# Kernel optimization log

Hardware: AMD Instinct MI355X
Metric: run time of the kernel (lower is better)

The kernel has to match this reference:

```python
import jax, jax.numpy as jnp
import numpy as np
from jax import lax

E = 8      # embed dim
H = 8      # num heads (head_dim = 1)
EPS = 1e-5


def pe_row(pos, d=E):
    # PositionalEncoding quirk: original adds pe[:, x.size(1), :] -> a SINGLE row at index L.
    i = jnp.arange(0, d, 2, dtype=jnp.float32)
    div = jnp.exp(i * (-np.log(10000.0) / d))
    row = jnp.zeros((d,), jnp.float32)
    row = row.at[0::2].set(jnp.sin(pos * div))
    row = row.at[1::2].set(jnp.cos(pos * div))
    return row


def layernorm(x, g, b):
    mu = jnp.mean(x, axis=-1, keepdims=True)
    var = jnp.mean((x - mu) ** 2, axis=-1, keepdims=True)
    return (x - mu) / jnp.sqrt(var + EPS) * g + b


def mha(q, k, v, wi, bi, wo, bo):
    # torch nn.MultiheadAttention, batch_first, eval mode (dropout off)
    d = E // H
    qp = q @ wi[:E].T + bi[:E]
    kp = k @ wi[E:2 * E].T + bi[E:2 * E]
    vp = v @ wi[2 * E:].T + bi[2 * E:]
    sh = lambda x: x.reshape(x.shape[0], x.shape[1], H, d).transpose(0, 2, 1, 3)
    qh, kh, vh = sh(qp), sh(kp), sh(vp)
    scores = jnp.einsum('bhqd,bhkd->bhqk', qh, kh) / np.sqrt(d)
    attn = jax.nn.softmax(scores, axis=-1)
    o = jnp.einsum('bhqk,bhkd->bhqd', attn, vh)
    B, _, L, _ = o.shape
    o = o.transpose(0, 2, 1, 3).reshape(B, L, E)
    return o @ wo.T + bo


def conv1d_k1p1(x, w, b):
    # Conv1d kernel_size=1, padding=1 (conv_tgt branch), then permute to (B, L, C)
    y = lax.conv_general_dilated(x, w, (1,), [(1, 1)],
                                 dimension_numbers=('NCW', 'OIW', 'NCW'))
    return (y + b[None, :, None]).transpose(0, 2, 1)


def setup_inputs() -> dict:
    key = jax.random.key(0)
    ks = jax.random.split(key, 32)
    B = 8192
    r = lambda i, shape, s=0.05: jax.random.normal(ks[i], shape, jnp.float32) * s
    return {
        'eeg': jax.random.normal(ks[0], (B, 2, 20, 118), jnp.float32),
        'pupil': jax.random.normal(ks[1], (B, 2, 30), jnp.float32),
        'speech': jax.random.normal(ks[2], (B, 2, 30), jnp.float32),
        'action': jax.random.normal(ks[3], (B, 2, 30), jnp.float32),
        'location': jax.random.normal(ks[4], (B, 3, 30), jnp.float32),
        'tgt': jax.random.normal(ks[5], (B, 30), jnp.float32),
        'eeg_conv_w': r(6, (E, 2, 20, 2), 0.1), 'eeg_conv_b': r(7, (E,)),
        'psa_conv_w': r(8, (E, 2, 1), 0.3), 'psa_conv_b': r(9, (E,)),
        'loc_conv_w': r(10, (E, 3, 1), 0.3), 'loc_conv_b': r(11, (E,)),
        'tgt_conv_w': r(12, (E, 1, 1), 0.3), 'tgt_conv_b': r(13, (E,)),
        'norm_g': jnp.ones((E,), jnp.float32), 'norm_b': jnp.zeros((E,), jnp.float32),
        'cross_in_w': r(14, (3 * E, E), 0.3), 'cross_in_b': r(15, (3 * E,)),
        'cross_out_w': r(16, (E, E), 0.3), 'cross_out_b': r(17, (E,)),
        'self_in_w': r(18, (3 * E, E), 0.3), 'self_in_b': r(19, (3 * E,)),
        'self_out_w': r(20, (E, E), 0.3), 'self_out_b': r(21, (E,)),
        'out_in_w': r(22, (3 * E, E), 0.3), 'out_in_b': r(23, (3 * E,)),
        'out_out_w': r(24, (E, E), 0.3), 'out_out_b': r(25, (E,)),
        'fc1_w': r(26, (90, 256), 0.1), 'fc1_b': r(27, (90,)),
    }


def reference(eeg, pupil, speech, action, location, tgt,
              eeg_conv_w, eeg_conv_b, psa_conv_w, psa_conv_b,
              loc_conv_w, loc_conv_b, tgt_conv_w, tgt_conv_b,
              norm_g, norm_b,
              cross_in_w, cross_in_b, cross_out_w, cross_out_b,
              self_in_w, self_in_b, self_out_w, self_out_b,
              out_in_w, out_in_b, out_out_w, out_out_b,
              fc1_w, fc1_b):
    B = eeg.shape[0]
    # eeg conv2d: (B,2,20,118) -> (B,8,1,30) -> (B,30,8)
    e = lax.conv_general_dilated(eeg, eeg_conv_w, (1, 4), 'VALID',
                                 dimension_numbers=('NCHW', 'OIHW', 'NCHW'))
    e = (e + eeg_conv_b[None, :, None, None]).squeeze(2).transpose(0, 2, 1)
    # pupil/speech/action/location (raw len 30 -> conv_tgt branch -> seq 32)
    p = conv1d_k1p1(pupil, psa_conv_w, psa_conv_b)
    s = conv1d_k1p1(speech, psa_conv_w, psa_conv_b)
    a = conv1d_k1p1(action, psa_conv_w, psa_conv_b)
    l = conv1d_k1p1(location, loc_conv_w, loc_conv_b)
    # positional encoding adds single row pe[L]
    e = e + pe_row(30.0)
    p = p + pe_row(32.0)
    s = s + pe_row(32.0)
    a = a + pe_row(32.0)
    l = l + pe_row(32.0)

    cross = lambda q, kv: mha(q, kv, kv, cross_in_w, cross_in_b, cross_out_w, cross_out_b)
    selfa = lambda x: mha(x, x, x, self_in_w, self_in_b, self_out_w, self_out_b)
    nrm = lambda x: layernorm(x, norm_g, norm_b)

    eeg_final = (nrm(cross(e, p)) + nrm(cross(e, a)) + nrm(cross(e, l))
                 + nrm(selfa(e)) + nrm(cross(e, s)))
    pupil_final = (nrm(cross(p, e)) + nrm(cross(p, a)) + nrm(cross(p, l))
                   + nrm(selfa(p)) + nrm(cross(p, s)))
    s_cross_l = nrm(cross(s, l))
    speech_final = (nrm(cross(s, e)) + nrm(cross(s, p)) + nrm(cross(s, a))
                    + s_cross_l)  # original omits speech_self
    # original bug: action_cross_location = norm(speech_cross_location)
    action_final = (nrm(cross(a, e)) + nrm(cross(a, p)) + s_cross_l
                    + nrm(selfa(a)) + nrm(cross(a, s)))
    concatenated = jnp.concatenate([eeg_final, pupil_final, action_final, speech_final], axis=1)  # (B,126,8)

    t = conv1d_k1p1(tgt[:, None, :], tgt_conv_w, tgt_conv_b)  # (B,32,8)
    t = t + pe_row(32.0)
    out = mha(t, concatenated, concatenated, out_in_w, out_in_b, out_out_w, out_out_b)  # (B,32,8)
    out = out.reshape(B, 32 * E) @ fc1_w.T + fc1_b  # (B,90)
    out = out.reshape(B, 30, 3).transpose(0, 2, 1)  # (B,3,30)
    return jax.nn.softmax(out, axis=1)
```

## Files before the change

### kernel.cpp

```cpp
#include <hip/hip_runtime.h>
#include <cstdint>
#include <cstddef>

#define NT 256
#define LOG2E 1.4426950408889634f

typedef float v2f __attribute__((ext_vector_type(2)));
typedef float v4f __attribute__((ext_vector_type(4)));

#if defined(__has_builtin)
#  if __has_builtin(__builtin_amdgcn_exp2f)
#    define EXP2F(x) __builtin_amdgcn_exp2f(x)
#  else
#    define EXP2F(x) exp2f(x)
#  endif
#else
#  define EXP2F(x) exp2f(x)
#endif

enum {
  OFF_EEGB = 0,
  OFF_PSAW = 8,
  OFF_PSAB = 24,
  OFF_LOCW = 32,
  OFF_LOCB = 56,
  OFF_TGTW = 64,
  OFF_TGTB = 72,
  OFF_NG   = 80,
  OFF_NB   = 88,
  OFF_CINW = 96,
  OFF_CINB = 288,
  OFF_COUTW= 312,
  OFF_COUTB= 376,
  OFF_SINW = 384,
  OFF_SINB = 576,
  OFF_SOUTW= 600,
  OFF_SOUTB= 664,
  OFF_OINW = 672,
  OFF_OINB = 864,
  OFF_OOUTW= 888,
  OFF_OOUTB= 952,
  OFF_FC1B = 960,
  OFF_PE30 = 1052,
  OFF_PE32 = 1060,
  OFF_Ebuf = 1068,
  OFF_Pbuf = 1308,
  OFF_Sbuf = 1564,
  OFF_Abuf = 1820,
  OFF_Lbuf = 2076,
  OFF_Tbuf = 2332,
  OFF_CAT  = 2588,
  OFF_QP   = 3596,
  OFF_K8   = 4236,
  OFF_V8   = 6540,
  OFF_FCO  = 8844,
  SM_TOTAL = 8936,
  OFF_EEGW = OFF_K8,
  OFF_KF   = OFF_K8,
  OFF_VF   = OFF_K8 + 1056,
};


__device__ __forceinline__ float grp8_sum(float v) {
  v += __shfl_xor(v, 1);
  v += __shfl_xor(v, 2);
  v += __shfl_xor(v, 4);
  return v;
}

__device__ __forceinline__ float dot8(const float* __restrict__ x,
                                      const float* __restrict__ w, float bias) {
  v4f xa = *(const v4f*)x, xb = *(const v4f*)(x + 4);
  v4f p = xa * *(const v4f*)w;
  p += xb * *(const v4f*)(w + 4);
  v2f q = p.xy + p.zw;
  return bias + q.x + q.y;
}

template<int LK>
__device__ __forceinline__ void kvproj(int set, int src, int winO, int binO,
                                       float* __restrict__ sm, int tid) {
  if (tid < LK * 8) {
    int r = tid >> 3, hh = tid & 7;
    const float* x = sm + src + r * 8;
    float kk = dot8(x, sm + winO + 64 + hh * 8, sm[binO + 8 + hh]);
    float vv = dot8(x, sm + winO + 128 + hh * 8, sm[binO + 16 + hh]);
    sm[OFF_K8 + set * 288 + hh * 36 + r] = kk;
    sm[OFF_V8 + set * 288 + hh * 36 + r] = vv;
  }
}

template<int LK>
__device__ __forceinline__ float attn_nv(float q, int qi, int h, int set,
                                         int woutO, int boutO, float* __restrict__ sm) {
  const float* Kp = sm + OFF_K8 + set * 288 + h * 36;
  const float* Vp = sm + OFF_V8 + set * 288 + h * 36;
  v4f l4 = {0.f,0.f,0.f,0.f}, A4 = {0.f,0.f,0.f,0.f};
  #pragma unroll
  for (int t = 0; t < (LK >> 2); t++) {
    v4f kk = *(const v4f*)(Kp + 4 * t);
    v4f vv = *(const v4f*)(Vp + 4 * t);
    v4f sc = kk * q;
    v4f ee = { EXP2F(sc.x), EXP2F(sc.y), EXP2F(sc.z), EXP2F(sc.w) };
    l4 += ee; A4 += ee * vv;
  }
  if constexpr ((LK & 3) != 0) {
    v2f kk = *(const v2f*)(Kp + (LK & ~3));
    v2f vv = *(const v2f*)(Vp + (LK & ~3));
    v2f sc = kk * q;
    v2f ee = { EXP2F(sc.x), EXP2F(sc.y) };
    l4.xy = l4.xy + ee; A4.xy = A4.xy + ee * vv;
  }
  v2f lp = l4.xy + l4.zw, ap = A4.xy + A4.zw;
  float ov = (ap.x + ap.y) * __builtin_amdgcn_rcpf(lp.x + lp.y);
  sm[OFF_QP + qi * 20 + h] = ov;
  float a = dot8(sm + OFF_QP + qi * 20, sm + woutO + h * 8, sm[boutO + h]);
  float mu = grp8_sum(a) * 0.125f;
  float dd = a - mu;
  return fmaf(dd * rsqrtf(grp8_sum(dd * dd) * 0.125f + 1e-5f),
              sm[OFF_NG + h], sm[OFF_NB + h]);
}

__global__ __launch_bounds__(NT, 4) void cmt_kernel(
    const float* __restrict__ eeg, const float* __restrict__ pupil,
    const float* __restrict__ speech, const float* __restrict__ action,
    const float* __restrict__ location, const float* __restrict__ tgt,
    const float* __restrict__ eeg_w, const float* __restrict__ eeg_b,
    const float* __restrict__ psa_w, const float* __restrict__ psa_b,
    const float* __restrict__ loc_w, const float* __restrict__ loc_b,
    const float* __restrict__ tgt_w, const float* __restrict__ tgt_b,
    const float* __restrict__ ng, const float* __restrict__ nb,
    const float* __restrict__ cin_w, const float* __restrict__ cin_b,
    const float* __restrict__ cout_w, const float* __restrict__ cout_b,
    const float* __restrict__ sin_w, const float* __restrict__ sin_b,
    const float* __restrict__ sout_w, const float* __restrict__ sout_b,
    const float* __restrict__ oin_w, const float* __restrict__ oin_b,
    const float* __restrict__ oout_w, const float* __restrict__ oout_b,
    const float* __restrict__ fc1_w, const float* __restrict__ fc1_b,
    float* __restrict__ out)
{
  __shared__ __align__(16) float sm[SM_TOTAL];
  const int tid = threadIdx.x;
  const int b = blockIdx.x;

#define CP(off, p, n) for (int i = tid; i < (n); i += NT) sm[(off)+i] = (p)[i]
#define CPQ(off, p, n, nq) for (int i = tid; i < (n); i += NT) sm[(off)+i] = (p)[i] * ((i < (nq)) ? LOG2E : 1.0f)

  for (int i = tid; i < 640; i += NT) sm[OFF_EEGW + (i / 80) * 84 + (i % 80)] = eeg_w[i];
  CP(OFF_EEGB, eeg_b, 8);
  CP(OFF_PSAW, psa_w, 16);   CP(OFF_PSAB, psa_b, 8);
  CP(OFF_LOCW, loc_w, 24);   CP(OFF_LOCB, loc_b, 8);
  CP(OFF_TGTW, tgt_w, 8);    CP(OFF_TGTB, tgt_b, 8);
  CP(OFF_NG, ng, 8);         CP(OFF_NB, nb, 8);
  CPQ(OFF_CINW, cin_w, 192, 64);  CPQ(OFF_CINB, cin_b, 24, 8);
  CP(OFF_COUTW, cout_w, 64); CP(OFF_COUTB, cout_b, 8);
  CPQ(OFF_SINW, sin_w, 192, 64);  CPQ(OFF_SINB, sin_b, 24, 8);
  CP(OFF_SOUTW, sout_w, 64); CP(OFF_SOUTB, sout_b, 8);
  CPQ(OFF_OINW, oin_w, 192, 64);  CPQ(OFF_OINB, oin_b, 24, 8);
  CP(OFF_OOUTW, oout_w, 64); CP(OFF_OOUTB, oout_b, 8);
  CP(OFF_FC1B, fc1_b, 90);
  if (tid < 16) {
    const float divs[4] = {1.f, 0.1f, 0.01f, 0.001f};
    float pos = (tid < 8) ? 30.f : 32.f;
    int e = tid & 7;
    float x = pos * divs[e >> 1];
    float v = (e & 1) ? cosf(x) : sinf(x);
    sm[((tid < 8) ? OFF_PE30 : OFF_PE32) + e] = v;
  }
  __syncthreads();

  if (tid < 240) {
    int w = tid >> 3, o = tid & 7;
    const float* ep = eeg + (size_t)b * 4720 + 4 * w;
    const float* wr = sm + OFF_EEGW + o * 84;
    v4f acc4 = {0.f, 0.f, 0.f, 0.f};
    #pragma unroll
    for (int t = 0; t < 20; t++) {
      int ik0 = 2 * t, ik1 = 2 * t + 1;
      float2 x0 = *(const float2*)(ep + (ik0 / 20) * 2360 + (ik0 % 20) * 118);
      float2 x1 = *(const float2*)(ep + (ik1 / 20) * 2360 + (ik1 % 20) * 118);
      v4f xv = {x0.x, x0.y, x1.x, x1.y};
      acc4 += xv * *(const v4f*)(wr + 4 * t);
    }
    v2f s2 = acc4.xy + acc4.zw;
    sm[OFF_Ebuf + w * 8 + o] = s2.x + s2.y + sm[OFF_EEGB + o] + sm[OFF_PE30 + o];
  }
  {
    int t = tid >> 3, o = tid & 7;
    bool inb = (t >= 1 && t <= 30);
    int ti = t - 1;
    float pe = sm[OFF_PE32 + o];
    float w0 = sm[OFF_PSAW + 2 * o], w1 = sm[OFF_PSAW + 2 * o + 1];
    float pb = sm[OFF_PSAB + o];
    float vp = pb, vs = pb, va = pb;
    float vl = sm[OFF_LOCB + o], vt = sm[OFF_TGTB + o];
    if (inb) {
      const float* pp = pupil    + (size_t)b * 60 + ti;
      const float* sp = speech   + (size_t)b * 60 + ti;
      const float* ap = action   + (size_t)b * 60 + ti;
      const float* lp = location + (size_t)b * 90 + ti;
      vp = fmaf(pp[0], w0, fmaf(pp[30], w1, vp));
      vs = fmaf(sp[0], w0, fmaf(sp[30], w1, vs));
      va = fmaf(ap[0], w0, fmaf(ap[30], w1, va));
      vl = fmaf(lp[0],  sm[OFF_LOCW + 3 * o],     vl);
      vl = fmaf(lp[30], sm[OFF_LOCW + 3 * o + 1], vl);
      vl = fmaf(lp[60], sm[OFF_LOCW + 3 * o + 2], vl);
      vt = fmaf(tgt[(size_t)b * 30 + ti], sm[OFF_TGTW + o], vt);
    }
    sm[OFF_Pbuf + tid] = vp + pe;
    sm[OFF_Sbuf + tid] = vs + pe;
    sm[OFF_Abuf + tid] = va + pe;
    sm[OFF_Lbuf + tid] = vl + pe;
    sm[OFF_Tbuf + tid] = vt + pe;
  }
  __syncthreads();

  kvproj<30>(0, OFF_Ebuf, OFF_CINW, OFF_CINB, sm, tid);
  kvproj<32>(1, OFF_Pbuf, OFF_CINW, OFF_CINB, sm, tid);
  kvproj<32>(2, OFF_Sbuf, OFF_CINW, OFF_CINB, sm, tid);
  kvproj<32>(3, OFF_Abuf, OFF_CINW, OFF_CINB, sm, tid);
  kvproj<32>(4, OFF_Lbuf, OFF_CINW, OFF_CINB, sm, tid);
  kvproj<30>(5, OFF_Ebuf, OFF_SINW, OFF_SINB, sm, tid);
  kvproj<32>(6, OFF_Pbuf, OFF_SINW, OFF_SINB, sm, tid);
  kvproj<32>(7, OFF_Abuf, OFF_SINW, OFF_SINB, sm, tid);
  __syncthreads();

  const int qi = tid >> 3, h = tid & 7;
  float carry;
  {
    if (qi < 30) {
      const float* xr = sm + OFF_Ebuf + qi * 8;
      float qc = dot8(xr, sm + OFF_CINW + h * 8, sm[OFF_CINB + h]);
      float qs = dot8(xr, sm + OFF_SINW + h * 8, sm[OFF_SINB + h]);
      float cat = attn_nv<32>(qc, qi, h, 1, OFF_COUTW, OFF_COUTB, sm)
                + attn_nv<32>(qc, qi, h, 3, OFF_COUTW, OFF_COUTB, sm)
                + attn_nv<32>(qc, qi, h, 4, OFF_COUTW, OFF_COUTB, sm)
                + attn_nv<30>(qs, qi, h, 5, OFF_SOUTW, OFF_SOUTB, sm)
                + attn_nv<32>(qc, qi, h, 2, OFF_COUTW, OFF_COUTB, sm);
      sm[OFF_CAT + qi * 8 + h] = cat;
    }
    {
      const float* xr = sm + OFF_Pbuf + qi * 8;
      float qc = dot8(xr, sm + OFF_CINW + h * 8, sm[OFF_CINB + h]);
      float qs = dot8(xr, sm + OFF_SINW + h * 8, sm[OFF_SINB + h]);
      float cat = attn_nv<30>(qc, qi, h, 0, OFF_COUTW, OFF_COUTB, sm)
                + attn_nv<32>(qc, qi, h, 3, OFF_COUTW, OFF_COUTB, sm)
                + attn_nv<32>(qc, qi, h, 4, OFF_COUTW, OFF_COUTB, sm)
                + attn_nv<32>(qs, qi, h, 6, OFF_SOUTW, OFF_SOUTB, sm)
                + attn_nv<32>(qc, qi, h, 2, OFF_COUTW, OFF_COUTB, sm);
      sm[OFF_CAT + (30 + qi) * 8 + h] = cat;
    }
    {
      const float* xr = sm + OFF_Sbuf + qi * 8;
      float qc = dot8(xr, sm + OFF_CINW + h * 8, sm[OFF_CINB + h]);
      float n1 = attn_nv<30>(qc, qi, h, 0, OFF_COUTW, OFF_COUTB, sm);
      float n2 = attn_nv<32>(qc, qi, h, 1, OFF_COUTW, OFF_COUTB, sm);
      float n3 = attn_nv<32>(qc, qi, h, 3, OFF_COUTW, OFF_COUTB, sm);
      carry    = attn_nv<32>(qc, qi, h, 4, OFF_COUTW, OFF_COUTB, sm);
      sm[OFF_CAT + (94 + qi) * 8 + h] = n1 + n2 + n3 + carry;
    }
    {
      const float* xr = sm + OFF_Abuf + qi * 8;
      float qc = dot8(xr, sm + OFF_CINW + h * 8, sm[OFF_CINB + h]);
      float qs = dot8(xr, sm + OFF_SINW + h * 8, sm[OFF_SINB + h]);
      float cat = attn_nv<30>(qc, qi, h, 0, OFF_COUTW, OFF_COUTB, sm)
                + attn_nv<32>(qc, qi, h, 1, OFF_COUTW, OFF_COUTB, sm)
                + carry
                + attn_nv<32>(qs, qi, h, 7, OFF_SOUTW, OFF_SOUTB, sm)
                + attn_nv<32>(qc, qi, h, 2, OFF_COUTW, OFF_COUTB, sm);
      sm[OFF_CAT + (62 + qi) * 8 + h] = cat;
    }
  }
  __syncthreads();

  for (int j = tid; j < 1008; j += NT) {
    int r = j >> 3, hh = j & 7;
    const float* x = sm + OFF_CAT + r * 8;
    float kk = dot8(x, sm + OFF_OINW + 64 + hh * 8, sm[OFF_OINB + 8 + hh]);
    float vv = dot8(x, sm + OFF_OINW + 128 + hh * 8, sm[OFF_OINB + 16 + hh]);
    sm[OFF_KF + hh * 132 + r] = kk;
    sm[OFF_VF + hh * 132 + r] = vv;
  }
  __syncthreads();

  {
    float qf = dot8(sm + OFF_Tbuf + qi * 8, sm + OFF_OINW + h * 8, sm[OFF_OINB + h]);
    const float* Kp = sm + OFF_KF + h * 132;
    const float* Vp = sm + OFF_VF + h * 132;
    v4f l4 = {0.f,0.f,0.f,0.f}, A4 = {0.f,0.f,0.f,0.f};
    #pragma unroll
    for (int t = 0; t < 31; t++) {
      v4f kk = *(const v4f*)(Kp + 4 * t);
      v4f vv = *(const v4f*)(Vp + 4 * t);
      v4f sc = kk * qf;
      v4f ee = { EXP2F(sc.x), EXP2F(sc.y), EXP2F(sc.z), EXP2F(sc.w) };
      l4 += ee; A4 += ee * vv;
    }
    {
      v2f kk = *(const v2f*)(Kp + 124);
      v2f vv = *(const v2f*)(Vp + 124);
      v2f sc = kk * qf;
      v2f ee = { EXP2F(sc.x), EXP2F(sc.y) };
      l4.xy = l4.xy + ee; A4.xy = A4.xy + ee * vv;
    }
    v2f lp = l4.xy + l4.zw, ap = A4.xy + A4.zw;
    float ov = (ap.x + ap.y) * __builtin_amdgcn_rcpf(lp.x + lp.y);
    sm[OFF_QP + qi * 20 + h] = ov;
    float a = dot8(sm + OFF_QP + qi * 20, sm + OFF_OOUTW + h * 8, sm[OFF_OOUTB + h]);
    sm[OFF_Tbuf + qi * 8 + h] = a;
  }
  __syncthreads();

  if (tid < 180) {
    int j = tid >> 1, p = tid & 1;
    const v4f* w4 = (const v4f*)(fc1_w + j * 256);
    const v4f* o4 = (const v4f*)(sm + OFF_Tbuf);
    v4f acc4 = {0.f, 0.f, 0.f, 0.f};
    #pragma unroll 8
    for (int c = p; c < 64; c += 2) acc4 += o4[c] * w4[c];
    v2f a2 = acc4.xy + acc4.zw;
    float acc = a2.x + a2.y;
    acc += __shfl_xor(acc, 1);
    if (p == 0) sm[OFF_FCO + j] = acc + sm[OFF_FC1B + j];
  }
  __syncthreads();
  if (tid < 30) {
    float x0 = sm[OFF_FCO + 3 * tid], x1 = sm[OFF_FCO + 3 * tid + 1], x2 = sm[OFF_FCO + 3 * tid + 2];
    float m = fmaxf(x0, fmaxf(x1, x2));
    float e0 = __expf(x0 - m), e1 = __expf(x1 - m), e2 = __expf(x2 - m);
    float inv = __builtin_amdgcn_rcpf(e0 + e1 + e2);
    float* op = out + (size_t)b * 90;
    op[tid]      = e0 * inv;
    op[30 + tid] = e1 * inv;
    op[60 + tid] = e2 * inv;
  }
#undef CP
#undef CPQ
}

extern "C" void kernel_launch(void* const* d_in, const int* in_sizes, int n_in,
                              void* d_out, int out_size, void* d_ws, size_t ws_size,
                              hipStream_t stream) {
  (void)n_in; (void)out_size; (void)d_ws; (void)ws_size;
  int B = in_sizes[0] / 4720;
  cmt_kernel<<<B, NT, 0, stream>>>(
      (const float*)d_in[0],  (const float*)d_in[1],  (const float*)d_in[2],
      (const float*)d_in[3],  (const float*)d_in[4],  (const float*)d_in[5],
      (const float*)d_in[6],  (const float*)d_in[7],  (const float*)d_in[8],
      (const float*)d_in[9],  (const float*)d_in[10], (const float*)d_in[11],
      (const float*)d_in[12], (const float*)d_in[13], (const float*)d_in[14],
      (const float*)d_in[15], (const float*)d_in[16], (const float*)d_in[17],
      (const float*)d_in[18], (const float*)d_in[19], (const float*)d_in[20],
      (const float*)d_in[21], (const float*)d_in[22], (const float*)d_in[23],
      (const float*)d_in[24], (const float*)d_in[25], (const float*)d_in[26],
      (const float*)d_in[27], (const float*)d_in[28], (const float*)d_in[29],
      (float*)d_out);
}
```

Measured before the change: 251.0 us.

## Process two queries per thread to share K/V loads across attention blocks

```diff
diff --git a/kernel.cpp b/kernel.cpp
--- a/kernel.cpp
+++ b/kernel.cpp
@@ -60,65 +60,63 @@
   OFF_VF   = OFF_K8 + 1056,
 };
 
-
-__device__ __forceinline__ float grp8_sum(float v) {
-  v += __shfl_xor(v, 1);
-  v += __shfl_xor(v, 2);
-  v += __shfl_xor(v, 4);
-  return v;
+__device__ __forceinline__ float hsum4(v4f a) {
+  v2f t = a.xy + a.zw;
+  return t.x + t.y;
 }
 
-__device__ __forceinline__ float dot8(const float* __restrict__ x,
-                                      const float* __restrict__ w, float bias) {
-  v4f xa = *(const v4f*)x, xb = *(const v4f*)(x + 4);
-  v4f p = xa * *(const v4f*)w;
-  p += xb * *(const v4f*)(w + 4);
-  v2f q = p.xy + p.zw;
-  return bias + q.x + q.y;
-}
-
 template<int LK>
-__device__ __forceinline__ void kvproj(int set, int src, int winO, int binO,
-                                       float* __restrict__ sm, int tid) {
-  if (tid < LK * 8) {
-    int r = tid >> 3, hh = tid & 7;
-    const float* x = sm + src + r * 8;
-    float kk = dot8(x, sm + winO + 64 + hh * 8, sm[binO + 8 + hh]);
-    float vv = dot8(x, sm + winO + 128 + hh * 8, sm[binO + 16 + hh]);
-    sm[OFF_K8 + set * 288 + hh * 36 + r] = kk;
-    sm[OFF_V8 + set * 288 + hh * 36 + r] = vv;
-  }
-}
-
-template<int LK>
-__device__ __forceinline__ float attn_nv(float q, int qi, int h, int set,
-                                         int woutO, int boutO, float* __restrict__ sm) {
-  const float* Kp = sm + OFF_K8 + set * 288 + h * 36;
-  const float* Vp = sm + OFF_V8 + set * 288 + h * 36;
-  v4f l4 = {0.f,0.f,0.f,0.f}, A4 = {0.f,0.f,0.f,0.f};
+__device__ __forceinline__ void attn2_core(float q1, float q2,
+                                           const float* Kp, const float* Vp,
+                                           float& ov1, float& ov2) {
+  v4f la = {0.f,0.f,0.f,0.f}, Aa = la, lb = la, Ab = la;
   #pragma unroll
   for (int t = 0; t < (LK >> 2); t++) {
     v4f kk = *(const v4f*)(Kp + 4 * t);
     v4f vv = *(const v4f*)(Vp + 4 * t);
-    v4f sc = kk * q;
-    v4f ee = { EXP2F(sc.x), EXP2F(sc.y), EXP2F(sc.z), EXP2F(sc.w) };
-    l4 += ee; A4 += ee * vv;
+    v4f s1 = kk * q1, s2 = kk * q2;
+    v4f e1 = { EXP2F(s1.x), EXP2F(s1.y), EXP2F(s1.z), EXP2F(s1.w) };
+    v4f e2 = { EXP2F(s2.x), EXP2F(s2.y), EXP2F(s2.z), EXP2F(s2.w) };
+    la += e1; Aa += e1 * vv;
+    lb += e2; Ab += e2 * vv;
   }
   if constexpr ((LK & 3) != 0) {
     v2f kk = *(const v2f*)(Kp + (LK & ~3));
     v2f vv = *(const v2f*)(Vp + (LK & ~3));
-    v2f sc = kk * q;
-    v2f ee = { EXP2F(sc.x), EXP2F(sc.y) };
-    l4.xy = l4.xy + ee; A4.xy = A4.xy + ee * vv;
-  }
-  v2f lp = l4.xy + l4.zw, ap = A4.xy + A4.zw;
-  float ov = (ap.x + ap.y) * __builtin_amdgcn_rcpf(lp.x + lp.y);
-  sm[OFF_QP + qi * 20 + h] = ov;
-  float a = dot8(sm + OFF_QP + qi * 20, sm + woutO + h * 8, sm[boutO + h]);
-  float mu = grp8_sum(a) * 0.125f;
-  float dd = a - mu;
-  return fmaf(dd * rsqrtf(grp8_sum(dd * dd) * 0.125f + 1e-5f),
-              sm[OFF_NG + h], sm[OFF_NB + h]);
+    v2f s1 = kk * q1, s2 = kk * q2;
+    v2f e1 = { EXP2F(s1.x), EXP2F(s1.y) };
+    v2f e2 = { EXP2F(s2.x), EXP2F(s2.y) };
+    la.xy = la.xy + e1; Aa.xy = Aa.xy + e1 * vv;
+    lb.xy = lb.xy + e2; Ab.xy = Ab.xy + e2 * vv;
+  }
+  ov1 = hsum4(Aa) * __builtin_amdgcn_rcpf(hsum4(la));
+  ov2 = hsum4(Ab) * __builtin_amdgcn_rcpf(hsum4(lb));
+}
+
+template<int LK>
+__device__ __forceinline__ void attn2_nv(float q1, float q2,
+                                         const float* Kp, const float* Vp,
+                                         float* qslot, int h,
+                                         v4f woa, v4f wob, float bo, float gg, float bb,
+                                         float& nv1, float& nv2) {
+  float ov1, ov2;
+  attn2_core<LK>(q1, q2, Kp, Vp, ov1, ov2);
+  qslot[h] = ov1; qslot[8 + h] = ov2;
+  v4f c0 = *(const v4f*)qslot,       c1 = *(const v4f*)(qslot + 4);
+  v4f d0 = *(const v4f*)(qslot + 8), d1 = *(const v4f*)(qslot + 12);
+  float a1 = bo + hsum4(c0 * woa + c1 * wob);
+  float a2 = bo + hsum4(d0 * woa + d1 * wob);
+  qslot[h] = a1; qslot[8 + h] = a2;
+  c0 = *(const v4f*)qslot;       c1 = *(const v4f*)(qslot + 4);
+  d0 = *(const v4f*)(qslot + 8); d1 = *(const v4f*)(qslot + 12);
+  float mu1 = hsum4(c0 + c1) * 0.125f;
+  float mu2 = hsum4(d0 + d1) * 0.125f;
+  v4f e0 = c0 - mu1, e1v = c1 - mu1;
+  v4f f0 = d0 - mu2, f1v = d1 - mu2;
+  float var1 = hsum4(e0 * e0 + e1v * e1v) * 0.125f;
+  float var2 = hsum4(f0 * f0 + f1v * f1v) * 0.125f;
+  nv1 = fmaf((a1 - mu1) * rsqrtf(var1 + 1e-5f), gg, bb);
+  nv2 = fmaf((a2 - mu2) * rsqrtf(var2 + 1e-5f), gg, bb);
 }
 
 __global__ __launch_bounds__(NT, 4) void cmt_kernel(
@@ -215,99 +213,177 @@
   }
   __syncthreads();
 
-  kvproj<30>(0, OFF_Ebuf, OFF_CINW, OFF_CINB, sm, tid);
-  kvproj<32>(1, OFF_Pbuf, OFF_CINW, OFF_CINB, sm, tid);
-  kvproj<32>(2, OFF_Sbuf, OFF_CINW, OFF_CINB, sm, tid);
-  kvproj<32>(3, OFF_Abuf, OFF_CINW, OFF_CINB, sm, tid);
-  kvproj<32>(4, OFF_Lbuf, OFF_CINW, OFF_CINB, sm, tid);
-  kvproj<30>(5, OFF_Ebuf, OFF_SINW, OFF_SINB, sm, tid);
-  kvproj<32>(6, OFF_Pbuf, OFF_SINW, OFF_SINB, sm, tid);
-  kvproj<32>(7, OFF_Abuf, OFF_SINW, OFF_SINB, sm, tid);
-  __syncthreads();
-
-  const int qi = tid >> 3, h = tid & 7;
-  float carry;
+  const int g = tid >> 3, h = tid & 7;
+  float* qslot = sm + OFF_QP + g * 20;
+
   {
-    if (qi < 30) {
-      const float* xr = sm + OFF_Ebuf + qi * 8;
-      float qc = dot8(xr, sm + OFF_CINW + h * 8, sm[OFF_CINB + h]);
-      float qs = dot8(xr, sm + OFF_SINW + h * 8, sm[OFF_SINB + h]);
-      float cat = attn_nv<32>(qc, qi, h, 1, OFF_COUTW, OFF_COUTB, sm)
-                + attn_nv<32>(qc, qi, h, 3, OFF_COUTW, OFF_COUTB, sm)
-                + attn_nv<32>(qc, qi, h, 4, OFF_COUTW, OFF_COUTB, sm)
-                + attn_nv<30>(qs, qi, h, 5, OFF_SOUTW, OFF_SOUTB, sm)
-                + attn_nv<32>(qc, qi, h, 2, OFF_COUTW, OFF_COUTB, sm);
-      sm[OFF_CAT + qi * 8 + h] = cat;
+    const int r = g;
+    v4f cka = *(const v4f*)(sm + OFF_CINW + 64 + h * 8), ckb = *(const v4f*)(sm + OFF_CINW + 68 + h * 8);
+    v4f cva = *(const v4f*)(sm + OFF_CINW + 128 + h * 8), cvb = *(const v4f*)(sm + OFF_CINW + 132 + h * 8);
+    float cbk = sm[OFF_CINB + 8 + h], cbv = sm[OFF_CINB + 16 + h];
+#define KV1(srcO, set, wka, wkb, wva, wvb, bk, bv) { \
+    v4f xa = *(const v4f*)(sm + (srcO) + r * 8); \
+    v4f xb = *(const v4f*)(sm + (srcO) + r * 8 + 4); \
+    sm[OFF_K8 + (set) * 288 + h * 36 + r] = (bk) + hsum4(xa * (wka) + xb * (wkb)); \
+    sm[OFF_V8 + (set) * 288 + h * 36 + r] = (bv) + hsum4(xa * (wva) + xb * (wvb)); }
+    if (r < 30) KV1(OFF_Ebuf, 0, cka, ckb, cva, cvb, cbk, cbv);
+    KV1(OFF_Pbuf, 1, cka, ckb, cva, cvb, cbk, cbv);
+    KV1(OFF_Sbuf, 2, cka, ckb, cva, cvb, cbk, cbv);
+    KV1(OFF_Abuf, 3, cka, ckb, cva, cvb, cbk, cbv);
+    KV1(OFF_Lbuf, 4, cka, ckb, cva, cvb, cbk, cbv);
+    v4f ska = *(const v4f*)(sm + OFF_SINW + 64 + h * 8), skb = *(const v4f*)(sm + OFF_SINW + 68 + h * 8);
+    v4f sva = *(const v4f*)(sm + OFF_SINW + 128 + h * 8), svb = *(const v4f*)(sm + OFF_SINW + 132 + h * 8);
+    float sbk = sm[OFF_SINB + 8 + h], sbv = sm[OFF_SINB + 16 + h];
+    if (r < 30) KV1(OFF_Ebuf, 5, ska, skb, sva, svb, sbk, sbv);
+    KV1(OFF_Pbuf, 6, ska, skb, sva, svb, sbk, sbv);
+    KV1(OFF_Abuf, 7, ska, skb, sva, svb, sbk, sbv);
+#undef KV1
+  }
+  __syncthreads();
+
+#define KSET(s) (sm + OFF_K8 + (s) * 288 + h * 36)
+#define VSET(s) (sm + OFF_V8 + (s) * 288 + h * 36)
+  {
+    v4f qwc_a = *(const v4f*)(sm + OFF_CINW + h * 8), qwc_b = *(const v4f*)(sm + OFF_CINW + h * 8 + 4);
+    v4f woc_a = *(const v4f*)(sm + OFF_COUTW + h * 8), woc_b = *(const v4f*)(sm + OFF_COUTW + h * 8 + 4);
+    float bqc = sm[OFF_CINB + h], boc = sm[OFF_COUTB + h];
+    float gg = sm[OFF_NG + h], bb = sm[OFF_NB + h];
+    float t1, t2;
+
+    if (g < 16) {
+      {
+        const float* x1 = sm + OFF_Ebuf + g * 8;
+        const float* x2 = sm + OFF_Ebuf + ((g < 14) ? (g + 16) : 13) * 8;
+        v4f x1a = *(const v4f*)x1, x1b = *(const v4f*)(x1 + 4);
+        v4f x2a = *(const v4f*)x2, x2b = *(const v4f*)(x2 + 4);
+        float qc1 = bqc + hsum4(x1a * qwc_a + x1b * qwc_b);
+        float qc2 = bqc + hsum4(x2a * qwc_a + x2b * qwc_b);
+        float cat1, cat2;
+        attn2_nv<32>(qc1, qc2, KSET(1), VSET(1), qslot, h, woc_a, woc_b, boc, gg, bb, cat1, cat2);
+        attn2_nv<32>(qc1, qc2, KSET(3), VSET(3), qslot, h, woc_a, woc_b, boc, gg, bb, t1, t2);
+        cat1 += t1; cat2 += t2;
+        attn2_nv<32>(qc1, qc2, KSET(4), VSET(4), qslot, h, woc_a, woc_b, boc, gg, bb, t1, t2);
+        cat1 += t1; cat2 += t2;
+        {
+          v4f qws_a = *(const v4f*)(sm + OFF_SINW + h * 8), qws_b = *(const v4f*)(sm + OFF_SINW + h * 8 + 4);
+          v4f wos_a = *(const v4f*)(sm + OFF_SOUTW + h * 8), wos_b = *(const v4f*)(sm + OFF_SOUTW + h * 8 + 4);
+          float qs1 = sm[OFF_SINB + h] + hsum4(x1a * qws_a + x1b * qws_b);
+          float qs2 = sm[OFF_SINB + h] + hsum4(x2a * qws_a + x2b * qws_b);
+          attn2_nv<30>(qs1, qs2, KSET(5), VSET(5), qslot, h, wos_a, wos_b, sm[OFF_SOUTB + h], gg, bb, t1, t2);
+          cat1 += t1; cat2 += t2;
+        }
+        attn2_nv<32>(qc1, qc2, KSET(2), VSET(2), qslot, h, woc_a, woc_b, boc, gg, bb, t1, t2);
+        cat1 += t1; cat2 += t2;
+        sm[OFF_CAT + g * 8 + h] = cat1;
+        if (g < 14) sm[OFF_CAT + (g + 16) * 8 + h] = cat2;
+      }
+      {
+        const float* x1 = sm + OFF_Pbuf + g * 8;
+        const float* x2 = sm + OFF_Pbuf + (g + 16) * 8;
+        v4f x1a = *(const v4f*)x1, x1b = *(const v4f*)(x1 + 4);
+        v4f x2a = *(const v4f*)x2, x2b = *(const v4f*)(x2 + 4);
+        float qc1 = bqc + hsum4(x1a * qwc_a + x1b * qwc_b);
+        float qc2 = bqc + hsum4(x2a * qwc_a + x2b * qwc_b);
+        float cat1, cat2;
+        attn2_nv<30>(qc1, qc2, KSET(0), VSET(0), qslot, h, woc_a, woc_b, boc, gg, bb, cat1, cat2);
+        attn2_nv<32>(qc1, qc2, KSET(3), VSET(3), qslot, h, woc_a, woc_b, boc, gg, bb, t1, t2);
+        cat1 += t1; cat2 += t2;
+        attn2_nv<32>(qc1, qc2, KSET(4), VSET(4), qslot, h, woc_a, woc_b, boc, gg, bb, t1, t2);
+        cat1 += t1; cat2 += t2;
+        {
+          v4f qws_a = *(const v4f*)(sm + OFF_SINW + h * 8), qws_b = *(const v4f*)(sm + OFF_SINW + h * 8 + 4);
+          v4f wos_a = *(const v4f*)(sm + OFF_SOUTW + h * 8), wos_b = *(const v4f*)(sm + OFF_SOUTW + h * 8 + 4);
+          float qs1 = sm[OFF_SINB + h] + hsum4(x1a * qws_a + x1b * qws_b);
+          float qs2 = sm[OFF_SINB + h] + hsum4(x2a * qws_a + x2b * qws_b);
+          attn2_nv<32>(qs1, qs2, KSET(6), VSET(6), qslot, h, wos_a, wos_b, sm[OFF_SOUTB + h], gg, bb, t1, t2);
+          cat1 += t1; cat2 += t2;
+        }
+        attn2_nv<32>(qc1, qc2, KSET(2), VSET(2), qslot, h, woc_a, woc_b, boc, gg, bb, t1, t2);
+        cat1 += t1; cat2 += t2;
+        sm[OFF_CAT + (30 + g) * 8 + h] = cat1;
+        sm[OFF_CAT + (30 + g + 16) * 8 + h] = cat2;
+      }
+    } else {
+      const int gq = g - 16;
+      float car1, car2;
+      {
+        const float* x1 = sm + OFF_Sbuf + gq * 8;
+        const float* x2 = sm + OFF_Sbuf + (gq + 16) * 8;
+        v4f x1a = *(const v4f*)x1, x1b = *(const v4f*)(x1 + 4);
+        v4f x2a = *(const v4f*)x2, x2b = *(const v4f*)(x2 + 4);
+        float qc1 = bqc + hsum4(x1a * qwc_a + x1b * qwc_b);
+        float qc2 = bqc + hsum4(x2a * qwc_a + x2b * qwc_b);
+        float cat1, cat2;
+        attn2_nv<30>(qc1, qc2, KSET(0), VSET(0), qslot, h, woc_a, woc_b, boc, gg, bb, cat1, cat2);
+        attn2_nv<32>(qc1, qc2, KSET(1), VSET(1), qslot, h, woc_a, woc_b, boc, gg, bb, t1, t2);
+        cat1 += t1; cat2 += t2;
+        attn2_nv<32>(qc1, qc2, KSET(3), VSET(3), qslot, h, woc_a, woc_b, boc, gg, bb, t1, t2);
+        cat1 += t1; cat2 += t2;
+        attn2_nv<32>(qc1, qc2, KSET(4), VSET(4), qslot, h, woc_a, woc_b, boc, gg, bb, car1, car2);
+        sm[OFF_CAT + (94 + gq) * 8 + h] = cat1 + car1;
+        sm[OFF_CAT + (94 + gq + 16) * 8 + h] = cat2 + car2;
+      }
+      {
+        const float* x1 = sm + OFF_Abuf + gq * 8;
+        const float* x2 = sm + OFF_Abuf + (gq + 16) * 8;
+        v4f x1a = *(const v4f*)x1, x1b = *(const v4f*)(x1 + 4);
+        v4f x2a = *(const v4f*)x2, x2b = *(const v4f*)(x2 + 4);
+        float qc1 = bqc + hsum4(x1a * qwc_a + x1b * qwc_b);
+        float qc2 = bqc + hsum4(x2a * qwc_a + x2b * qwc_b);
+        float cat1, cat2;
+        attn2_nv<30>(qc1, qc2, KSET(0), VSET(0), qslot, h, woc_a, woc_b, boc, gg, bb, cat1, cat2);
+        attn2_nv<32>(qc1, qc2, KSET(1), VSET(1), qslot, h, woc_a, woc_b, boc, gg, bb, t1, t2);
+        cat1 += t1 + car1; cat2 += t2 + car2;
+        {
+          v4f qws_a = *(const v4f*)(sm + OFF_SINW + h * 8), qws_b = *(const v4f*)(sm + OFF_SINW + h * 8 + 4);
+          v4f wos_a = *(const v4f*)(sm + OFF_SOUTW + h * 8), wos_b = *(const v4f*)(sm + OFF_SOUTW + h * 8 + 4);
+          float qs1 = sm[OFF_SINB + h] + hsum4(x1a * qws_a + x1b * qws_b);
+          float qs2 = sm[OFF_SINB + h] + hsum4(x2a * qws_a + x2b * qws_b);
+          attn2_nv<32>(qs1, qs2, KSET(7), VSET(7), qslot, h, wos_a, wos_b, sm[OFF_SOUTB + h], gg, bb, t1, t2);
+          cat1 += t1; cat2 += t2;
+        }
+        attn2_nv<32>(qc1, qc2, KSET(2), VSET(2), qslot, h, woc_a, woc_b, boc, gg, bb, t1, t2);
+        cat1 += t1; cat2 += t2;
+        sm[OFF_CAT + (62 + gq) * 8 + h] = cat1;
+        sm[OFF_CAT + (62 + gq + 16) * 8 + h] = cat2;
+      }
     }
-    {
-      const float* xr = sm + OFF_Pbuf + qi * 8;
-      float qc = dot8(xr, sm + OFF_CINW + h * 8, sm[OFF_CINB + h]);
-      float qs = dot8(xr, sm + OFF_SINW + h * 8, sm[OFF_SINB + h]);
-      float cat = attn_nv<30>(qc, qi, h, 0, OFF_COUTW, OFF_COUTB, sm)
-                + attn_nv<32>(qc, qi, h, 3, OFF_COUTW, OFF_COUTB, sm)
-                + attn_nv<32>(qc, qi, h, 4, OFF_COUTW, OFF_COUTB, sm)
-                + attn_nv<32>(qs, qi, h, 6, OFF_SOUTW, OFF_SOUTB, sm)
-                + attn_nv<32>(qc, qi, h, 2, OFF_COUTW, OFF_COUTB, sm);
-      sm[OFF_CAT + (30 + qi) * 8 + h] = cat;
+  }
+#undef KSET
+#undef VSET
+  __syncthreads();
+
+  {
+    v4f fka = *(const v4f*)(sm + OFF_OINW + 64 + h * 8), fkb = *(const v4f*)(sm + OFF_OINW + 68 + h * 8);
+    v4f fva = *(const v4f*)(sm + OFF_OINW + 128 + h * 8), fvb = *(const v4f*)(sm + OFF_OINW + 132 + h * 8);
+    float fbk = sm[OFF_OINB + 8 + h], fbv = sm[OFF_OINB + 16 + h];
+    for (int r = g; r < 126; r += 32) {
+      v4f xa = *(const v4f*)(sm + OFF_CAT + r * 8);
+      v4f xb = *(const v4f*)(sm + OFF_CAT + r * 8 + 4);
+      sm[OFF_KF + h * 132 + r] = fbk + hsum4(xa * fka + xb * fkb);
+      sm[OFF_VF + h * 132 + r] = fbv + hsum4(xa * fva + xb * fvb);
     }
-    {
-      const float* xr = sm + OFF_Sbuf + qi * 8;
-      float qc = dot8(xr, sm + OFF_CINW + h * 8, sm[OFF_CINB + h]);
-      float n1 = attn_nv<30>(qc, qi, h, 0, OFF_COUTW, OFF_COUTB, sm);
-      float n2 = attn_nv<32>(qc, qi, h, 1, OFF_COUTW, OFF_COUTB, sm);
-      float n3 = attn_nv<32>(qc, qi, h, 3, OFF_COUTW, OFF_COUTB, sm);
-      carry    = attn_nv<32>(qc, qi, h, 4, OFF_COUTW, OFF_COUTB, sm);
-      sm[OFF_CAT + (94 + qi) * 8 + h] = n1 + n2 + n3 + carry;
-    }
-    {
-      const float* xr = sm + OFF_Abuf + qi * 8;
-      float qc = dot8(xr, sm + OFF_CINW + h * 8, sm[OFF_CINB + h]);
-      float qs = dot8(xr, sm + OFF_SINW + h * 8, sm[OFF_SINB + h]);
-      float cat = attn_nv<30>(qc, qi, h, 0, OFF_COUTW, OFF_COUTB, sm)
-                + attn_nv<32>(qc, qi, h, 1, OFF_COUTW, OFF_COUTB, sm)
-                + carry
-                + attn_nv<32>(qs, qi, h, 7, OFF_SOUTW, OFF_SOUTB, sm)
-                + attn_nv<32>(qc, qi, h, 2, OFF_COUTW, OFF_COUTB, sm);
-      sm[OFF_CAT + (62 + qi) * 8 + h] = cat;
-    }
-  }
-  __syncthreads();
-
-  for (int j = tid; j < 1008; j += NT) {
-    int r = j >> 3, hh = j & 7;
-    const float* x = sm + OFF_CAT + r * 8;
-    float kk = dot8(x, sm + OFF_OINW + 64 + hh * 8, sm[OFF_OINB + 8 + hh]);
-    float vv = dot8(x, sm + OFF_OINW + 128 + hh * 8, sm[OFF_OINB + 16 + hh]);
-    sm[OFF_KF + hh * 132 + r] = kk;
-    sm[OFF_VF + hh * 132 + r] = vv;
-  }
-  __syncthreads();
-
-  {
-    float qf = dot8(sm + OFF_Tbuf + qi * 8, sm + OFF_OINW + h * 8, sm[OFF_OINB + h]);
-    const float* Kp = sm + OFF_KF + h * 132;
-    const float* Vp = sm + OFF_VF + h * 132;
-    v4f l4 = {0.f,0.f,0.f,0.f}, A4 = {0.f,0.f,0.f,0.f};
-    #pragma unroll
-    for (int t = 0; t < 31; t++) {
-      v4f kk = *(const v4f*)(Kp + 4 * t);
-      v4f vv = *(const v4f*)(Vp + 4 * t);
-      v4f sc = kk * qf;
-      v4f ee = { EXP2F(sc.x), EXP2F(sc.y), EXP2F(sc.z), EXP2F(sc.w) };
-      l4 += ee; A4 += ee * vv;
-    }
-    {
-      v2f kk = *(const v2f*)(Kp + 124);
-      v2f vv = *(const v2f*)(Vp + 124);
-      v2f sc = kk * qf;
-      v2f ee = { EXP2F(sc.x), EXP2F(sc.y) };
-      l4.xy = l4.xy + ee; A4.xy = A4.xy + ee * vv;
-    }
-    v2f lp = l4.xy + l4.zw, ap = A4.xy + A4.zw;
-    float ov = (ap.x + ap.y) * __builtin_amdgcn_rcpf(lp.x + lp.y);
-    sm[OFF_QP + qi * 20 + h] = ov;
-    float a = dot8(sm + OFF_QP + qi * 20, sm + OFF_OOUTW + h * 8, sm[OFF_OOUTB + h]);
-    sm[OFF_Tbuf + qi * 8 + h] = a;
+  }
+  __syncthreads();
+
+  if (g >= 16) {
+    const int gq = g - 16;
+    const float* x1 = sm + OFF_Tbuf + gq * 8;
+    const float* x2 = sm + OFF_Tbuf + (gq + 16) * 8;
+    v4f qwf_a = *(const v4f*)(sm + OFF_OINW + h * 8), qwf_b = *(const v4f*)(sm + OFF_OINW + h * 8 + 4);
+    v4f x1a = *(const v4f*)x1, x1b = *(const v4f*)(x1 + 4);
+    v4f x2a = *(const v4f*)x2, x2b = *(const v4f*)(x2 + 4);
+    float qf1 = sm[OFF_OINB + h] + hsum4(x1a * qwf_a + x1b * qwf_b);
+    float qf2 = sm[OFF_OINB + h] + hsum4(x2a * qwf_a + x2b * qwf_b);
+    float ov1, ov2;
+    attn2_core<126>(qf1, qf2, sm + OFF_KF + h * 132, sm + OFF_VF + h * 132, ov1, ov2);
+    qslot[h] = ov1; qslot[8 + h] = ov2;
+    v4f c0 = *(const v4f*)qslot,       c1 = *(const v4f*)(qslot + 4);
+    v4f d0 = *(const v4f*)(qslot + 8), d1 = *(const v4f*)(qslot + 12);
+    v4f wfo_a = *(const v4f*)(sm + OFF_OOUTW + h * 8), wfo_b = *(const v4f*)(sm + OFF_OOUTW + h * 8 + 4);
+    float bfo = sm[OFF_OOUTB + h];
+    sm[OFF_Tbuf + gq * 8 + h]        = bfo + hsum4(c0 * wfo_a + c1 * wfo_b);
+    sm[OFF_Tbuf + (gq + 16) * 8 + h] = bfo + hsum4(d0 * wfo_a + d1 * wfo_b);
   }
   __syncthreads();
 
@@ -318,8 +394,7 @@
     v4f acc4 = {0.f, 0.f, 0.f, 0.f};
     #pragma unroll 8
     for (int c = p; c < 64; c += 2) acc4 += o4[c] * w4[c];
-    v2f a2 = acc4.xy + acc4.zw;
-    float acc = a2.x + a2.y;
+    float acc = hsum4(acc4);
     acc += __shfl_xor(acc, 1);
     if (p == 0) sm[OFF_FCO + j] = acc + sm[OFF_FC1B + j];
   }
```

New measurement: 256.1 us. 2.0% more time.
